# Performance work log

Measured on AMD Instinct MI355X. Metric: run time of the kernel, lower is better.

Reference implementation:

```python
import jax, jax.numpy as jnp
import numpy as np

EPS = 1e-5
TOP_K = 3
W_THRESH = 0.01

def _bn(x, g, b):
    # training-mode batch norm over (N,H,W) per channel
    m = x.mean(axis=(0, 2, 3), keepdims=True)
    v = x.var(axis=(0, 2, 3), keepdims=True)
    return (x - m) * jax.lax.rsqrt(v + EPS) * g[None, :, None, None] + b[None, :, None, None]

def _conv(x, w, stride=1, pad=0, dil=1, groups=1):
    return jax.lax.conv_general_dilated(
        x, w, (stride, stride), [(pad, pad), (pad, pad)],
        rhs_dilation=(dil, dil),
        dimension_numbers=("NCHW", "OIHW", "NCHW"),
        feature_group_count=groups)

def _maxpool3(x):
    return jax.lax.reduce_window(x, -jnp.inf, jax.lax.max, (1, 1, 3, 3), (1, 1, 1, 1),
                                 [(0, 0), (0, 0), (1, 1), (1, 1)])

def _avgpool3(x):
    s = jax.lax.reduce_window(x, 0.0, jax.lax.add, (1, 1, 3, 3), (1, 1, 1, 1),
                              [(0, 0), (0, 0), (1, 1), (1, 1)])
    return s / 9.0  # count_include_pad=True as in torch avg_pool2d

def setup_inputs() -> dict:
    key = jax.random.key(0)
    ks = jax.random.split(key, 16)
    Cin, C = 128, 256
    B, H, W = 64, 32, 32
    f = lambda k, shp, s=0.05: jax.random.normal(k, shp, dtype=jnp.float32) * s
    gamma = lambda k, n: 1.0 + 0.1 * jax.random.normal(k, (n,), dtype=jnp.float32)
    return {
        "x": jax.random.normal(ks[0], (B, Cin, H, W), dtype=jnp.float32),
        "arch_weights": jax.random.normal(ks[1], (8,), dtype=jnp.float32),
        "w_in": f(ks[2], (C, Cin, 1, 1)),
        "g_in": gamma(ks[3], C), "b_in": jnp.zeros((C,), jnp.float32),
        "w3": f(ks[4], (C, C, 3, 3)),
        "g3": gamma(ks[5], C), "b3": jnp.zeros((C,), jnp.float32),
        "w5": f(ks[6], (C, C, 5, 5)),
        "g5": gamma(ks[7], C), "b5": jnp.zeros((C,), jnp.float32),
        "w_dw": f(ks[8], (C, 1, 3, 3), 0.2),
        "w_pw": f(ks[9], (C, C, 1, 1)),
        "gs": gamma(ks[10], C), "bs": jnp.zeros((C,), jnp.float32),
        "wd": f(ks[11], (C, C, 3, 3)),
        "gd": gamma(ks[12], C), "bd": jnp.zeros((C,), jnp.float32),
        "gmp": gamma(ks[13], C), "bmp": jnp.zeros((C,), jnp.float32),
        "gap": gamma(ks[14], C), "bap": jnp.zeros((C,), jnp.float32),
    }

def _forward(x, arch_weights, w_in, g_in, b_in, w3, g3, b3, w5, g5, b5,
             w_dw, w_pw, gs, bs, wd, gd, bd, gmp, bmp, gap, bap):
    # input transition: 1x1 conv -> BN -> ReLU (in_channels != out_channels)
    h = jax.nn.relu(_bn(_conv(x, w_in), g_in, b_in))
    # top-k thresholded renormalized mixture weights over 8 candidate ops
    w = jax.nn.softmax(arch_weights)
    tv, ti = jax.lax.top_k(w, TOP_K)
    sel = jnp.zeros_like(w).at[ti].set(tv)
    sel = jnp.where(sel >= W_THRESH, sel, 0.0)
    sel = sel / jnp.maximum(sel.sum(), 1e-12)
    r = jax.nn.relu(h)
    # op order: [none, max_pool_3x3, avg_pool_3x3, skip, conv_3x3, conv_5x5, sep_conv_3x3, dil_conv_3x3]
    out = sel[1] * _bn(_maxpool3(h), gmp, bmp)
    out = out + sel[2] * _bn(_avgpool3(h), gap, bap)
    out = out + sel[3] * h
    out = out + sel[4] * _bn(_conv(r, w3, pad=1), g3, b3)
    out = out + sel[5] * _bn(_conv(r, w5, pad=2), g5, b5)
    out = out + sel[6] * _bn(_conv(_conv(r, w_dw, pad=1, groups=r.shape[1]), w_pw), gs, bs)
    out = out + sel[7] * _bn(_conv(r, wd, pad=2, dil=2), gd, bd)
    return out

def reference(x, arch_weights, w_in, g_in, b_in, w3, g3, b3, w5, g5, b5,
              w_dw, w_pw, gs, bs, wd, gd, bd, gmp, bmp, gap, bap):
    return _forward(x, arch_weights, w_in, g_in, b_in, w3, g3, b3, w5, g5, b5,
                    w_dw, w_pw, gs, bs, wd, gd, bd, gmp, bmp, gap, bap)
```

## Files before the change

kernel.cpp:

```cpp
#include <hip/hip_runtime.h>

#define CIN_  128
#define C_    256
#define HW_   1024
#define NPC_  65536.0f
#define NB_   16384

constexpr size_t NELEM = 16777216ull;

__device__ float g_sel[8];
__device__ float g_stats[8 * 512];
__device__ int   g_isf32;
__device__ float g_h[NELEM];
__device__ float g_c3[NELEM];
__device__ float g_c5[NELEM];
__device__ float g_cd[NELEM];
__device__ float g_pm[NELEM];
__device__ float g_pa[NELEM];
__device__ float g_pw[NELEM];
__device__ float g_dw[NELEM];

__device__ float g_w5f[32 * 256 * 25 * 8];
__device__ float g_w3f[32 * 256 * 9 * 8];
__device__ float g_wdf[32 * 256 * 9 * 8];
__device__ float g_wtf[32 * 128 * 8];
__device__ float g_wpf[32 * 256 * 8];

__device__ __forceinline__ float u2f(unsigned short u) {
    union { unsigned int i; float f; } x; x.i = ((unsigned int)u) << 16; return x.f;
}
__device__ __forceinline__ unsigned short f2u(float f) {
    union { float f; unsigned int i; } x; x.f = f;
    unsigned int r = x.i + 0x7fffu + ((x.i >> 16) & 1u);
    return (unsigned short)(r >> 16);
}
__device__ __forceinline__ float ldq(const void* p, long i, int isf32) {
    return isf32 ? ((const float*)p)[i] : u2f(((const unsigned short*)p)[i]);
}

#define FMA8X4(acc, wq0, wq1, x0v, x1v, x2v, x3v)                                     \
    acc[0][0] += x0v*wq0.x; acc[0][1] += x1v*wq0.x; acc[0][2] += x2v*wq0.x; acc[0][3] += x3v*wq0.x; \
    acc[1][0] += x0v*wq0.y; acc[1][1] += x1v*wq0.y; acc[1][2] += x2v*wq0.y; acc[1][3] += x3v*wq0.y; \
    acc[2][0] += x0v*wq0.z; acc[2][1] += x1v*wq0.z; acc[2][2] += x2v*wq0.z; acc[2][3] += x3v*wq0.z; \
    acc[3][0] += x0v*wq0.w; acc[3][1] += x1v*wq0.w; acc[3][2] += x2v*wq0.w; acc[3][3] += x3v*wq0.w; \
    acc[4][0] += x0v*wq1.x; acc[4][1] += x1v*wq1.x; acc[4][2] += x2v*wq1.x; acc[4][3] += x3v*wq1.x; \
    acc[5][0] += x0v*wq1.y; acc[5][1] += x1v*wq1.y; acc[5][2] += x2v*wq1.y; acc[5][3] += x3v*wq1.y; \
    acc[6][0] += x0v*wq1.z; acc[6][1] += x1v*wq1.z; acc[6][2] += x2v*wq1.z; acc[6][3] += x3v*wq1.z; \
    acc[7][0] += x0v*wq1.w; acc[7][1] += x1v*wq1.w; acc[7][2] += x2v*wq1.w; acc[7][3] += x3v*wq1.w;

__global__ void k_prep(const void* __restrict__ x, const void* __restrict__ aw) {
    __shared__ int flag_s;
    __shared__ float red[256];
    const int t = threadIdx.x;
    for (int i = t; i < 8 * 512; i += 256) g_stats[i] = 0.f;
    const unsigned short* xu = (const unsigned short*)x;
    int bad = 0;
    for (int i = t; i < 8192; i += 256) {
        unsigned int e = (xu[i] >> 7) & 0xFFu;
        if (e >= 0xC6u) ++bad;
    }
    red[t] = (float)bad;
    __syncthreads();
    for (int off = 128; off > 0; off >>= 1) {
        if (t < off) red[t] += red[t + off];
        __syncthreads();
    }
    if (t == 0) { flag_s = (red[0] > 4.0f) ? 1 : 0; g_isf32 = flag_s; }
    __syncthreads();
    const int isf32 = flag_s;
    if (t == 0) {
        float w[8];
        float mx = -1e30f;
        for (int i = 0; i < 8; ++i) { w[i] = ldq(aw, i, isf32); mx = fmaxf(mx, w[i]); }
        float s = 0.f;
        for (int i = 0; i < 8; ++i) { w[i] = expf(w[i] - mx); s += w[i]; }
        for (int i = 0; i < 8; ++i) w[i] /= s;
        float sv[8] = {0,0,0,0,0,0,0,0};
        bool used[8] = {false,false,false,false,false,false,false,false};
        for (int k = 0; k < 3; ++k) {
            int bi = -1; float bv = -1.f;
            for (int i = 0; i < 8; ++i) if (!used[i] && w[i] > bv) { bv = w[i]; bi = i; }
            used[bi] = true; sv[bi] = bv;
        }
        float tot = 0.f;
        for (int i = 0; i < 8; ++i) { if (sv[i] < 0.01f) sv[i] = 0.f; tot += sv[i]; }
        tot = fmaxf(tot, 1e-12f);
        for (int i = 0; i < 8; ++i) g_sel[i] = sv[i] / tot;
    }
}

__global__ __launch_bounds__(256)
void k_wconv(const void* __restrict__ w3, const void* __restrict__ w5,
             const void* __restrict__ wd, const void* __restrict__ wi,
             const void* __restrict__ wp) {
    const int cg = blockIdx.x;
    const int t  = threadIdx.x;
    const int isf32 = g_isf32;
    for (int o = t; o < 51200; o += 256) {
        int u = o & 7, r = o >> 3, tap = r % 25, ci = r / 25;
        g_w5f[(size_t)cg * 51200 + o] =
            ldq(w5, ((long)(cg * 8 + u) * C_ + ci) * 25 + tap, isf32);
    }
    for (int o = t; o < 18432; o += 256) {
        int u = o & 7, r = o >> 3, tap = r % 9, ci = r / 9;
        long ii = ((long)(cg * 8 + u) * C_ + ci) * 9 + tap;
        g_w3f[(size_t)cg * 18432 + o] = ldq(w3, ii, isf32);
        g_wdf[(size_t)cg * 18432 + o] = ldq(wd, ii, isf32);
    }
    for (int o = t; o < 1024; o += 256) {
        int u = o & 7, ci = o >> 3;
        g_wtf[cg * 1024 + o] = ldq(wi, (long)(cg * 8 + u) * CIN_ + ci, isf32);
    }
    for (int o = t; o < 2048; o += 256) {
        int u = o & 7, ci = o >> 3;
        g_wpf[cg * 2048 + o] = ldq(wp, (long)(cg * 8 + u) * C_ + ci, isf32);
    }
}

__device__ __forceinline__ void stats_epilogue(float* red, float s, float s2,
                                               int t, int c, int slot) {
    __syncthreads();
    red[t] = s; red[t + 256] = s2;
    __syncthreads();
    for (int off = 128; off > 0; off >>= 1) {
        if (t < off) { red[t] += red[t + off]; red[t + 256] += red[t + 256 + off]; }
        __syncthreads();
    }
    if (t == 0) {
        atomicAdd(&g_stats[slot * 512 + c], red[0]);
        atomicAdd(&g_stats[slot * 512 + 256 + c], red[256]);
    }
}

__device__ __forceinline__ void stats_ep2(float* red, int t,
                                          float sA, float s2A, float sB, float s2B,
                                          int cA, int cB, int slot) {
    __syncthreads();
    red[t] = sA; red[t + 256] = s2A; red[t + 512] = sB; red[t + 768] = s2B;
    __syncthreads();
    for (int off = 128; off > 0; off >>= 1) {
        if (t < off) {
            red[t]       += red[t + off];
            red[t + 256] += red[t + 256 + off];
            red[t + 512] += red[t + 512 + off];
            red[t + 768] += red[t + 768 + off];
        }
        __syncthreads();
    }
    if (t == 0) {
        atomicAdd(&g_stats[slot * 512 + cA],       red[0]);
        atomicAdd(&g_stats[slot * 512 + 256 + cA], red[256]);
        atomicAdd(&g_stats[slot * 512 + cB],       red[512]);
        atomicAdd(&g_stats[slot * 512 + 256 + cB], red[768]);
    }
}

__device__ __forceinline__ void stats_all8(float* red, int t, float acc[8][4],
                                           int c0, int slot) {
    #pragma unroll
    for (int u = 0; u < 8; u += 2)
        stats_ep2(red, t,
            acc[u][0]+acc[u][1]+acc[u][2]+acc[u][3],
            acc[u][0]*acc[u][0]+acc[u][1]*acc[u][1]+acc[u][2]*acc[u][2]+acc[u][3]*acc[u][3],
            acc[u+1][0]+acc[u+1][1]+acc[u+1][2]+acc[u+1][3],
            acc[u+1][0]*acc[u+1][0]+acc[u+1][1]*acc[u+1][1]+acc[u+1][2]*acc[u+1][2]+acc[u+1][3]*acc[u+1][3],
            c0 + u, c0 + u + 1, slot);
}

__global__ __launch_bounds__(256)
void k_trans(const void* __restrict__ xin) {
    __shared__ float red[1024];
    const int t  = threadIdx.x;
    const int cg = blockIdx.x & 31;
    const int c0 = cg * 8;
    const int b  = blockIdx.x >> 5;
    const float* wb = g_wtf + cg * 1024;
    float acc[8][4];
    #pragma unroll
    for (int k = 0; k < 8; ++k)
        #pragma unroll
        for (int j = 0; j < 4; ++j) acc[k][j] = 0.f;

    const size_t base0 = (size_t)b * CIN_ * 1024 + t;
    if (g_isf32) {
        const float* xf = (const float*)xin;
        for (int ci = 0; ci < CIN_; ++ci) {
            const float* xp = xf + base0 + (size_t)ci * 1024;
            float x0v = xp[0], x1v = xp[256], x2v = xp[512], x3v = xp[768];
            float4 wq0 = *(const float4*)(wb + ci * 8);
            float4 wq1 = *(const float4*)(wb + ci * 8 + 4);
            FMA8X4(acc, wq0, wq1, x0v, x1v, x2v, x3v)
        }
    } else {
        const unsigned short* xu = (const unsigned short*)xin;
        for (int ci = 0; ci < CIN_; ++ci) {
            const unsigned short* xp = xu + base0 + (size_t)ci * 1024;
            float x0v = u2f(xp[0]),   x1v = u2f(xp[256]);
            float x2v = u2f(xp[512]), x3v = u2f(xp[768]);
            float4 wq0 = *(const float4*)(wb + ci * 8);
            float4 wq1 = *(const float4*)(wb + ci * 8 + 4);
            FMA8X4(acc, wq0, wq1, x0v, x1v, x2v, x3v)
        }
    }
    #pragma unroll
    for (int k = 0; k < 8; ++k) {
        float* o = g_dw + (size_t)(b * C_ + c0 + k) * HW_;
        o[t] = acc[k][0]; o[t + 256] = acc[k][1];
        o[t + 512] = acc[k][2]; o[t + 768] = acc[k][3];
    }
    stats_all8(red, t, acc, c0, 0);
}

__global__ __launch_bounds__(256)
void k_bnrelu(const void* __restrict__ g, const void* __restrict__ bb) {
    size_t idx = ((size_t)blockIdx.x * 256 + threadIdx.x) * 4;
    int c = (int)((idx >> 10) & (C_ - 1));
    int isf32 = g_isf32;
    float mean = g_stats[c] * (1.0f / NPC_);
    float var  = g_stats[256 + c] * (1.0f / NPC_) - mean * mean;
    float rstd = rsqrtf(fmaxf(var, 0.f) + 1e-5f);
    float gv = ldq(g, c, isf32), bv = ldq(bb, c, isf32);
    float4 r = *(const float4*)(g_dw + idx);
    float4 h;
    h.x = fmaxf(0.f, (r.x - mean) * rstd * gv + bv);
    h.y = fmaxf(0.f, (r.y - mean) * rstd * gv + bv);
    h.z = fmaxf(0.f, (r.z - mean) * rstd * gv + bv);
    h.w = fmaxf(0.f, (r.w - mean) * rstd * gv + bv);
    *(float4*)(g_h + idx) = h;
}

__global__ __launch_bounds__(256)
void k_pool_fused() {
    const float s1 = g_sel[1], s2 = g_sel[2];
    if (s1 == 0.f && s2 == 0.f) return;
    __shared__ float xs[34 * 33];
    __shared__ float red[512];
    const int t = threadIdx.x;
    const int c = blockIdx.x & (C_ - 1);
    const int y  = t >> 3;
    const int x0 = (t & 7) * 4;
    const float* hp = g_h + (size_t)blockIdx.x * HW_;
    float4 r = *(const float4*)(hp + t * 4);
    float* xw = xs + y * 33 + x0;
    xw[0] = r.x; xw[1] = r.y; xw[2] = r.z; xw[3] = r.w;
    __syncthreads();
    float mx[4] = {0.f, 0.f, 0.f, 0.f};
    float sm[4] = {0.f, 0.f, 0.f, 0.f};
    #pragma unroll
    for (int ky = 0; ky < 3; ++ky) {
        int iy = y + ky - 1;
        if (iy < 0 || iy >= 32) continue;
        float row[6];
        #pragma unroll
        for (int i = 0; i < 6; ++i) {
            int ix = x0 + i - 1;
            row[i] = (ix >= 0 && ix < 32) ? xs[iy * 33 + ix] : 0.0f;
        }
        #pragma unroll
        for (int kx = 0; kx < 3; ++kx)
            #pragma unroll
            for (int j = 0; j < 4; ++j) {
                mx[j] = fmaxf(mx[j], row[j + kx]);
                sm[j] += row[j + kx];
            }
    }
    #pragma unroll
    for (int j = 0; j < 4; ++j) sm[j] *= (1.0f / 9.0f);
    const size_t ob = (size_t)blockIdx.x * HW_ + y * 32 + x0;
    if (s1 != 0.f) {
        float* o = g_pm + ob;
        o[0] = mx[0]; o[1] = mx[1]; o[2] = mx[2]; o[3] = mx[3];
        stats_epilogue(red, mx[0]+mx[1]+mx[2]+mx[3],
                       mx[0]*mx[0]+mx[1]*mx[1]+mx[2]*mx[2]+mx[3]*mx[3], t, c, 1);
    }
    if (s2 != 0.f) {
        float* o = g_pa + ob;
        o[0] = sm[0]; o[1] = sm[1]; o[2] = sm[2]; o[3] = sm[3];
        stats_epilogue(red, sm[0]+sm[1]+sm[2]+sm[3],
                       sm[0]*sm[0]+sm[1]*sm[1]+sm[2]*sm[2]+sm[3]*sm[3], t, c, 2);
    }
}

template<int KS, int DIL, int PAD, int SLOT>
__global__ __launch_bounds__(256)
void k_conv1() {
    if (g_sel[SLOT] == 0.0f) return;
    constexpr int TRW  = 8 + 2 * PAD;
    constexpr int TAPS = KS * KS;
    __shared__ float xs[4][2][TRW * 40];
    const int t  = threadIdx.x;
    const int w  = t >> 6;
    const int l  = t & 63;
    const int cg = blockIdx.x & 31;
    const int c0 = cg * 8;
    const int b  = blockIdx.x >> 5;
    const int y  = l >> 3;
    const int x0 = (l & 7) * 4;
    const int y0 = w * 8;
    const float* hb = g_h + (size_t)b * C_ * HW_;
    const float* wb = (SLOT == 4 ? g_w3f : SLOT == 5 ? g_w5f : g_wdf)
                      + (size_t)cg * (C_ * TAPS * 8);
    float* obuf = (SLOT == 4) ? g_c3 : (SLOT == 5) ? g_c5 : g_cd;

    const int grA = y0 - PAD + y;
    const bool okA = (grA >= 0) && (grA < 32);
    const int grB = grA + 8;
    const bool okB = (y < 2 * PAD) && (grB < 32);

    float acc[8][4];
    #pragma unroll
    for (int u = 0; u < 8; ++u)
        #pragma unroll
        for (int j = 0; j < 4; ++j) acc[u][j] = 0.f;

    {
        float* xw = &xs[w][0][0];
        for (int i = l; i < 2 * TRW * 40; i += 64) xw[i] = 0.f;
    }
    if (okA) *(float4*)(&xs[w][0][y * 40 + 4 + x0]) =
        *(const float4*)(hb + (size_t)grA * 32 + x0);
    if (okB) *(float4*)(&xs[w][0][(y + 8) * 40 + 4 + x0]) =
        *(const float4*)(hb + (size_t)grB * 32 + x0);
    int cur = 0;

    for (int ci = 0; ci < C_; ++ci) {
        float4 rA = {0.f,0.f,0.f,0.f}, rB = {0.f,0.f,0.f,0.f};
        if (ci + 1 < C_) {
            const float* hn = hb + (size_t)(ci + 1) * HW_;
            if (okA) rA = *(const float4*)(hn + grA * 32 + x0);
            if (okB) rB = *(const float4*)(hn + grB * 32 + x0);
        }
        const float* xsc = xs[w][cur];
        const float* wc  = wb + ci * (TAPS * 8);
        #pragma unroll
        for (int ky = 0; ky < KS; ++ky) {
            const int rr = (y + ky * DIL) * 40 + x0;
            float wnd[12];
            if (PAD == 1) {
                wnd[3] = xsc[rr + 3];
                float4 qb = *(const float4*)(xsc + rr + 4);
                wnd[4] = qb.x; wnd[5] = qb.y; wnd[6] = qb.z; wnd[7] = qb.w;
                wnd[8] = xsc[rr + 8];
            } else {
                float2 qa = *(const float2*)(xsc + rr + 2);
                float4 qb = *(const float4*)(xsc + rr + 4);
                float2 qc = *(const float2*)(xsc + rr + 8);
                wnd[2] = qa.x; wnd[3] = qa.y;
                wnd[4] = qb.x; wnd[5] = qb.y; wnd[6] = qb.z; wnd[7] = qb.w;
                wnd[8] = qc.x; wnd[9] = qc.y;
            }
            #pragma unroll
            for (int kx = 0; kx < KS; ++kx) {
                const float4 wA = *(const float4*)(wc + (ky * KS + kx) * 8);
                const float4 wB = *(const float4*)(wc + (ky * KS + kx) * 8 + 4);
                #pragma unroll
                for (int j = 0; j < 4; ++j) {
                    const float v = wnd[(4 - PAD) + j + kx * DIL];
                    acc[0][j] += v * wA.x; acc[1][j] += v * wA.y;
                    acc[2][j] += v * wA.z; acc[3][j] += v * wA.w;
                    acc[4][j] += v * wB.x; acc[5][j] += v * wB.y;
                    acc[6][j] += v * wB.z; acc[7][j] += v * wB.w;
                }
            }
        }
        if (ci + 1 < C_) {
            float* xn = xs[w][cur ^ 1];
            if (okA) *(float4*)(xn + y * 40 + 4 + x0) = rA;
            if (okB) *(float4*)(xn + (y + 8) * 40 + 4 + x0) = rB;
        }
        cur ^= 1;
    }

    #pragma unroll
    for (int u = 0; u < 8; ++u) {
        float4 o; o.x = acc[u][0]; o.y = acc[u][1]; o.z = acc[u][2]; o.w = acc[u][3];
        *(float4*)(obuf + (size_t)(b * C_ + c0 + u) * HW_ + (y0 + y) * 32 + x0) = o;
    }
    float* red = &xs[0][0][0];
    stats_all8(red, t, acc, c0, SLOT);
}

__global__ __launch_bounds__(256)
void k_dw(const void* __restrict__ wt) {
    if (g_sel[6] == 0.0f) return;
    __shared__ float xs[34 * 33];
    const int t = threadIdx.x;
    const int c = blockIdx.x & (C_ - 1);
    const int y  = t >> 3;
    const int x0 = (t & 7) * 4;
    const int isf32 = g_isf32;
    const float* hp = g_h + (size_t)blockIdx.x * HW_;
    float4 r = *(const float4*)(hp + t * 4);
    float* xw = xs + y * 33 + x0;
    xw[0] = r.x; xw[1] = r.y; xw[2] = r.z; xw[3] = r.w;
    __syncthreads();
    float wv[9];
    #pragma unroll
    for (int k = 0; k < 9; ++k) wv[k] = ldq(wt, (long)c * 9 + k, isf32);
    float acc[4] = {0.f, 0.f, 0.f, 0.f};
    #pragma unroll
    for (int ky = 0; ky < 3; ++ky) {
        int iy = y + ky - 1;
        if (iy < 0 || iy >= 32) continue;
        float row[6];
        #pragma unroll
        for (int i = 0; i < 6; ++i) {
            int ix = x0 + i - 1;
            row[i] = (ix >= 0 && ix < 32) ? xs[iy * 33 + ix] : 0.0f;
        }
        #pragma unroll
        for (int kx = 0; kx < 3; ++kx)
            #pragma unroll
            for (int j = 0; j < 4; ++j)
                acc[j] += row[j + kx] * wv[ky * 3 + kx];
    }
    float* o = g_dw + (size_t)blockIdx.x * HW_ + y * 32 + x0;
    o[0] = acc[0]; o[1] = acc[1]; o[2] = acc[2]; o[3] = acc[3];
}

__global__ __launch_bounds__(256)
void k_pw() {
    if (g_sel[6] == 0.0f) return;
    __shared__ float red[1024];
    const int t  = threadIdx.x;
    const int cg = blockIdx.x & 31;
    const int c0 = cg * 8;
    const int b  = blockIdx.x >> 5;
    const float* hb = g_dw + (size_t)b * C_ * HW_ + t;
    const float* wb = g_wpf + cg * 2048;
    float acc[8][4];
    #pragma unroll
    for (int k = 0; k < 8; ++k)
        #pragma unroll
        for (int j = 0; j < 4; ++j) acc[k][j] = 0.f;
    for (int ci = 0; ci < C_; ++ci) {
        const float* hp = hb + (size_t)ci * HW_;
        float x0v = hp[0], x1v = hp[256], x2v = hp[512], x3v = hp[768];
        float4 wq0 = *(const float4*)(wb + ci * 8);
        float4 wq1 = *(const float4*)(wb + ci * 8 + 4);
        FMA8X4(acc, wq0, wq1, x0v, x1v, x2v, x3v)
    }
    #pragma unroll
    for (int k = 0; k < 8; ++k) {
        float* o = g_pw + (size_t)(b * C_ + c0 + k) * HW_;
        o[t] = acc[k][0]; o[t + 256] = acc[k][1];
        o[t + 512] = acc[k][2]; o[t + 768] = acc[k][3];
    }
    stats_all8(red, t, acc, c0, 6);
}

__device__ __forceinline__ void bn_term(float4& o, const float* buf, size_t idx,
                                        int c, int slot, float sv,
                                        const void* g, const void* bb, int isf32) {
    float mean = g_stats[slot * 512 + c] * (1.0f / NPC_);
    float var  = g_stats[slot * 512 + 256 + c] * (1.0f / NPC_) - mean * mean;
    float rstd = rsqrtf(fmaxf(var, 0.f) + 1e-5f);
    float gv = ldq(g, c, isf32), bv = ldq(bb, c, isf32);
    float4 r = *(const float4*)(buf + idx);
    o.x += sv * ((r.x - mean) * rstd * gv + bv);
    o.y += sv * ((r.y - mean) * rstd * gv + bv);
    o.z += sv * ((r.z - mean) * rstd * gv + bv);
    o.w += sv * ((r.w - mean) * rstd * gv + bv);
}

__global__ __launch_bounds__(256)
void k_final_all(void* __restrict__ out,
                 const void* __restrict__ gmp, const void* __restrict__ bmp,
                 const void* __restrict__ gap, const void* __restrict__ bap,
                 const void* __restrict__ g3,  const void* __restrict__ b3,
                 const void* __restrict__ g5,  const void* __restrict__ b5,
                 const void* __restrict__ gs,  const void* __restrict__ bs,
                 const void* __restrict__ gd,  const void* __restrict__ bd) {
    size_t idx = ((size_t)blockIdx.x * 256 + threadIdx.x) * 4;
    int c = (int)((idx >> 10) & (C_ - 1));
    int isf32 = g_isf32;
    float4 o = {0.f, 0.f, 0.f, 0.f};
    float s3 = g_sel[3];
    if (s3 != 0.f) {
        float4 h = *(const float4*)(g_h + idx);
        o.x = s3 * h.x; o.y = s3 * h.y; o.z = s3 * h.z; o.w = s3 * h.w;
    }
    float sv;
    if ((sv = g_sel[1]) != 0.f) bn_term(o, g_pm, idx, c, 1, sv, gmp, bmp, isf32);
    if ((sv = g_sel[2]) != 0.f) bn_term(o, g_pa, idx, c, 2, sv, gap, bap, isf32);
    if ((sv = g_sel[4]) != 0.f) bn_term(o, g_c3, idx, c, 4, sv, g3,  b3,  isf32);
    if ((sv = g_sel[5]) != 0.f) bn_term(o, g_c5, idx, c, 5, sv, g5,  b5,  isf32);
    if ((sv = g_sel[6]) != 0.f) bn_term(o, g_pw, idx, c, 6, sv, gs,  bs,  isf32);
    if ((sv = g_sel[7]) != 0.f) bn_term(o, g_cd, idx, c, 7, sv, gd,  bd,  isf32);
    if (isf32) {
        *(float4*)((float*)out + idx) = o;
    } else {
        ushort4 u; u.x = f2u(o.x); u.y = f2u(o.y); u.z = f2u(o.z); u.w = f2u(o.w);
        *(ushort4*)((unsigned short*)out + idx) = u;
    }
}

extern "C" void kernel_launch(void* const* d_in, const int* in_sizes, int n_in,
                              void* d_out, int out_size, void* d_ws, size_t ws_size,
                              hipStream_t stream) {
    const void* x    = d_in[0];
    const void* aw   = d_in[1];
    const void* w_in = d_in[2];
    const void* g_in = d_in[3];
    const void* b_in = d_in[4];
    const void* w3   = d_in[5];
    const void* g3   = d_in[6];
    const void* b3   = d_in[7];
    const void* w5   = d_in[8];
    const void* g5   = d_in[9];
    const void* b5   = d_in[10];
    const void* wdw  = d_in[11];
    const void* wpw  = d_in[12];
    const void* gs   = d_in[13];
    const void* bs   = d_in[14];
    const void* wd   = d_in[15];
    const void* gd   = d_in[16];
    const void* bd   = d_in[17];
    const void* gmp  = d_in[18];
    const void* bmp  = d_in[19];
    const void* gap  = d_in[20];
    const void* bap  = d_in[21];

    dim3 Bk(256);
    dim3 Gfull(NB_);
    dim3 Gc8(2048);

    k_prep<<<dim3(1), Bk, 0, stream>>>(x, aw);
    k_wconv<<<dim3(32), Bk, 0, stream>>>(w3, w5, wd, w_in, wpw);

    k_trans<<<Gc8, Bk, 0, stream>>>(x);
    k_bnrelu<<<Gfull, Bk, 0, stream>>>(g_in, b_in);

    k_pool_fused<<<Gfull, Bk, 0, stream>>>();

    k_conv1<3, 1, 1, 4><<<Gc8, Bk, 0, stream>>>();
    k_conv1<5, 1, 2, 5><<<Gc8, Bk, 0, stream>>>();
    k_conv1<3, 2, 2, 7><<<Gc8, Bk, 0, stream>>>();

    k_dw<<<Gfull, Bk, 0, stream>>>(wdw);
    k_pw<<<Gc8, Bk, 0, stream>>>();

    k_final_all<<<Gfull, Bk, 0, stream>>>(d_out,
        gmp, bmp, gap, bap, g3, b3, g5, b5, gs, bs, gd, bd);
}
```

Before: 1.216 ms.

## Widen output-channel tile to 16 and fuse BN-ReLU, pooling and depthwise conv

Each block of the 1x1, 3x3, 5x5, dilated and pointwise convolutions now computes 16 output channels instead of 8. Weight repacking and grids are adjusted to match, so each loaded input value is reused across more channels. The BN+ReLU, pooling and depthwise kernels are merged into one per-channel kernel that keeps the activated plane in shared memory, removing two reloads of h and two launches. The wider tile doubles accumulator registers, which risks spills or lower occupancy, and halves the block count.

```diff
diff --git a/kernel.cpp b/kernel.cpp
--- a/kernel.cpp
+++ b/kernel.cpp
@@ -20,11 +20,11 @@
 __device__ float g_pw[NELEM];
 __device__ float g_dw[NELEM];
 
-__device__ float g_w5f[32 * 256 * 25 * 8];
-__device__ float g_w3f[32 * 256 * 9 * 8];
-__device__ float g_wdf[32 * 256 * 9 * 8];
-__device__ float g_wtf[32 * 128 * 8];
-__device__ float g_wpf[32 * 256 * 8];
+__device__ float g_w5f[16 * 256 * 25 * 16];
+__device__ float g_w3f[16 * 256 * 9 * 16];
+__device__ float g_wdf[16 * 256 * 9 * 16];
+__device__ float g_wtf[16 * 128 * 16];
+__device__ float g_wpf[16 * 256 * 16];
 
 __device__ __forceinline__ float u2f(unsigned short u) {
     union { unsigned int i; float f; } x; x.i = ((unsigned int)u) << 16; return x.f;
@@ -38,15 +38,23 @@
     return isf32 ? ((const float*)p)[i] : u2f(((const unsigned short*)p)[i]);
 }
 
-#define FMA8X4(acc, wq0, wq1, x0v, x1v, x2v, x3v)                                     \
-    acc[0][0] += x0v*wq0.x; acc[0][1] += x1v*wq0.x; acc[0][2] += x2v*wq0.x; acc[0][3] += x3v*wq0.x; \
-    acc[1][0] += x0v*wq0.y; acc[1][1] += x1v*wq0.y; acc[1][2] += x2v*wq0.y; acc[1][3] += x3v*wq0.y; \
-    acc[2][0] += x0v*wq0.z; acc[2][1] += x1v*wq0.z; acc[2][2] += x2v*wq0.z; acc[2][3] += x3v*wq0.z; \
-    acc[3][0] += x0v*wq0.w; acc[3][1] += x1v*wq0.w; acc[3][2] += x2v*wq0.w; acc[3][3] += x3v*wq0.w; \
-    acc[4][0] += x0v*wq1.x; acc[4][1] += x1v*wq1.x; acc[4][2] += x2v*wq1.x; acc[4][3] += x3v*wq1.x; \
-    acc[5][0] += x0v*wq1.y; acc[5][1] += x1v*wq1.y; acc[5][2] += x2v*wq1.y; acc[5][3] += x3v*wq1.y; \
-    acc[6][0] += x0v*wq1.z; acc[6][1] += x1v*wq1.z; acc[6][2] += x2v*wq1.z; acc[6][3] += x3v*wq1.z; \
-    acc[7][0] += x0v*wq1.w; acc[7][1] += x1v*wq1.w; acc[7][2] += x2v*wq1.w; acc[7][3] += x3v*wq1.w;
+#define FMA16X4(acc, wq0, wq1, wq2, wq3, x0v, x1v, x2v, x3v)                                             \
+    acc[ 0][0]+=x0v*wq0.x; acc[ 0][1]+=x1v*wq0.x; acc[ 0][2]+=x2v*wq0.x; acc[ 0][3]+=x3v*wq0.x;          \
+    acc[ 1][0]+=x0v*wq0.y; acc[ 1][1]+=x1v*wq0.y; acc[ 1][2]+=x2v*wq0.y; acc[ 1][3]+=x3v*wq0.y;          \
+    acc[ 2][0]+=x0v*wq0.z; acc[ 2][1]+=x1v*wq0.z; acc[ 2][2]+=x2v*wq0.z; acc[ 2][3]+=x3v*wq0.z;          \
+    acc[ 3][0]+=x0v*wq0.w; acc[ 3][1]+=x1v*wq0.w; acc[ 3][2]+=x2v*wq0.w; acc[ 3][3]+=x3v*wq0.w;          \
+    acc[ 4][0]+=x0v*wq1.x; acc[ 4][1]+=x1v*wq1.x; acc[ 4][2]+=x2v*wq1.x; acc[ 4][3]+=x3v*wq1.x;          \
+    acc[ 5][0]+=x0v*wq1.y; acc[ 5][1]+=x1v*wq1.y; acc[ 5][2]+=x2v*wq1.y; acc[ 5][3]+=x3v*wq1.y;          \
+    acc[ 6][0]+=x0v*wq1.z; acc[ 6][1]+=x1v*wq1.z; acc[ 6][2]+=x2v*wq1.z; acc[ 6][3]+=x3v*wq1.z;          \
+    acc[ 7][0]+=x0v*wq1.w; acc[ 7][1]+=x1v*wq1.w; acc[ 7][2]+=x2v*wq1.w; acc[ 7][3]+=x3v*wq1.w;          \
+    acc[ 8][0]+=x0v*wq2.x; acc[ 8][1]+=x1v*wq2.x; acc[ 8][2]+=x2v*wq2.x; acc[ 8][3]+=x3v*wq2.x;          \
+    acc[ 9][0]+=x0v*wq2.y; acc[ 9][1]+=x1v*wq2.y; acc[ 9][2]+=x2v*wq2.y; acc[ 9][3]+=x3v*wq2.y;          \
+    acc[10][0]+=x0v*wq2.z; acc[10][1]+=x1v*wq2.z; acc[10][2]+=x2v*wq2.z; acc[10][3]+=x3v*wq2.z;          \
+    acc[11][0]+=x0v*wq2.w; acc[11][1]+=x1v*wq2.w; acc[11][2]+=x2v*wq2.w; acc[11][3]+=x3v*wq2.w;          \
+    acc[12][0]+=x0v*wq3.x; acc[12][1]+=x1v*wq3.x; acc[12][2]+=x2v*wq3.x; acc[12][3]+=x3v*wq3.x;          \
+    acc[13][0]+=x0v*wq3.y; acc[13][1]+=x1v*wq3.y; acc[13][2]+=x2v*wq3.y; acc[13][3]+=x3v*wq3.y;          \
+    acc[14][0]+=x0v*wq3.z; acc[14][1]+=x1v*wq3.z; acc[14][2]+=x2v*wq3.z; acc[14][3]+=x3v*wq3.z;          \
+    acc[15][0]+=x0v*wq3.w; acc[15][1]+=x1v*wq3.w; acc[15][2]+=x2v*wq3.w; acc[15][3]+=x3v*wq3.w;
 
 __global__ void k_prep(const void* __restrict__ x, const void* __restrict__ aw) {
     __shared__ int flag_s;
@@ -96,24 +104,24 @@
     const int cg = blockIdx.x;
     const int t  = threadIdx.x;
     const int isf32 = g_isf32;
-    for (int o = t; o < 51200; o += 256) {
-        int u = o & 7, r = o >> 3, tap = r % 25, ci = r / 25;
-        g_w5f[(size_t)cg * 51200 + o] =
-            ldq(w5, ((long)(cg * 8 + u) * C_ + ci) * 25 + tap, isf32);
-    }
-    for (int o = t; o < 18432; o += 256) {
-        int u = o & 7, r = o >> 3, tap = r % 9, ci = r / 9;
-        long ii = ((long)(cg * 8 + u) * C_ + ci) * 9 + tap;
-        g_w3f[(size_t)cg * 18432 + o] = ldq(w3, ii, isf32);
-        g_wdf[(size_t)cg * 18432 + o] = ldq(wd, ii, isf32);
-    }
-    for (int o = t; o < 1024; o += 256) {
-        int u = o & 7, ci = o >> 3;
-        g_wtf[cg * 1024 + o] = ldq(wi, (long)(cg * 8 + u) * CIN_ + ci, isf32);
+    for (int o = t; o < 102400; o += 256) {
+        int u = o & 15, r = o >> 4, tap = r % 25, ci = r / 25;
+        g_w5f[(size_t)cg * 102400 + o] =
+            ldq(w5, ((long)(cg * 16 + u) * C_ + ci) * 25 + tap, isf32);
+    }
+    for (int o = t; o < 36864; o += 256) {
+        int u = o & 15, r = o >> 4, tap = r % 9, ci = r / 9;
+        long ii = ((long)(cg * 16 + u) * C_ + ci) * 9 + tap;
+        g_w3f[(size_t)cg * 36864 + o] = ldq(w3, ii, isf32);
+        g_wdf[(size_t)cg * 36864 + o] = ldq(wd, ii, isf32);
     }
     for (int o = t; o < 2048; o += 256) {
-        int u = o & 7, ci = o >> 3;
-        g_wpf[cg * 2048 + o] = ldq(wp, (long)(cg * 8 + u) * C_ + ci, isf32);
+        int u = o & 15, ci = o >> 4;
+        g_wtf[cg * 2048 + o] = ldq(wi, (long)(cg * 16 + u) * CIN_ + ci, isf32);
+    }
+    for (int o = t; o < 4096; o += 256) {
+        int u = o & 15, ci = o >> 4;
+        g_wpf[cg * 4096 + o] = ldq(wp, (long)(cg * 16 + u) * C_ + ci, isf32);
     }
 }
 
@@ -155,10 +163,10 @@
     }
 }
 
-__device__ __forceinline__ void stats_all8(float* red, int t, float acc[8][4],
-                                           int c0, int slot) {
-    #pragma unroll
-    for (int u = 0; u < 8; u += 2)
+__device__ __forceinline__ void stats_all16(float* red, int t, float acc[16][4],
+                                            int c0, int slot) {
+    #pragma unroll
+    for (int u = 0; u < 16; u += 2)
         stats_ep2(red, t,
             acc[u][0]+acc[u][1]+acc[u][2]+acc[u][3],
             acc[u][0]*acc[u][0]+acc[u][1]*acc[u][1]+acc[u][2]*acc[u][2]+acc[u][3]*acc[u][3],
@@ -171,13 +179,13 @@
 void k_trans(const void* __restrict__ xin) {
     __shared__ float red[1024];
     const int t  = threadIdx.x;
-    const int cg = blockIdx.x & 31;
-    const int c0 = cg * 8;
-    const int b  = blockIdx.x >> 5;
-    const float* wb = g_wtf + cg * 1024;
-    float acc[8][4];
-    #pragma unroll
-    for (int k = 0; k < 8; ++k)
+    const int cg = blockIdx.x & 15;
+    const int c0 = cg * 16;
+    const int b  = blockIdx.x >> 4;
+    const float* wb = g_wtf + cg * 2048;
+    float acc[16][4];
+    #pragma unroll
+    for (int k = 0; k < 16; ++k)
         #pragma unroll
         for (int j = 0; j < 4; ++j) acc[k][j] = 0.f;
 
@@ -187,9 +195,11 @@
         for (int ci = 0; ci < CIN_; ++ci) {
             const float* xp = xf + base0 + (size_t)ci * 1024;
             float x0v = xp[0], x1v = xp[256], x2v = xp[512], x3v = xp[768];
-            float4 wq0 = *(const float4*)(wb + ci * 8);
-            float4 wq1 = *(const float4*)(wb + ci * 8 + 4);
-            FMA8X4(acc, wq0, wq1, x0v, x1v, x2v, x3v)
+            float4 wq0 = *(const float4*)(wb + ci * 16);
+            float4 wq1 = *(const float4*)(wb + ci * 16 + 4);
+            float4 wq2 = *(const float4*)(wb + ci * 16 + 8);
+            float4 wq3 = *(const float4*)(wb + ci * 16 + 12);
+            FMA16X4(acc, wq0, wq1, wq2, wq3, x0v, x1v, x2v, x3v)
         }
     } else {
         const unsigned short* xu = (const unsigned short*)xin;
@@ -197,87 +207,112 @@
             const unsigned short* xp = xu + base0 + (size_t)ci * 1024;
             float x0v = u2f(xp[0]),   x1v = u2f(xp[256]);
             float x2v = u2f(xp[512]), x3v = u2f(xp[768]);
-            float4 wq0 = *(const float4*)(wb + ci * 8);
-            float4 wq1 = *(const float4*)(wb + ci * 8 + 4);
-            FMA8X4(acc, wq0, wq1, x0v, x1v, x2v, x3v)
-        }
-    }
-    #pragma unroll
-    for (int k = 0; k < 8; ++k) {
+            float4 wq0 = *(const float4*)(wb + ci * 16);
+            float4 wq1 = *(const float4*)(wb + ci * 16 + 4);
+            float4 wq2 = *(const float4*)(wb + ci * 16 + 8);
+            float4 wq3 = *(const float4*)(wb + ci * 16 + 12);
+            FMA16X4(acc, wq0, wq1, wq2, wq3, x0v, x1v, x2v, x3v)
+        }
+    }
+    #pragma unroll
+    for (int k = 0; k < 16; ++k) {
         float* o = g_dw + (size_t)(b * C_ + c0 + k) * HW_;
         o[t] = acc[k][0]; o[t + 256] = acc[k][1];
         o[t + 512] = acc[k][2]; o[t + 768] = acc[k][3];
     }
-    stats_all8(red, t, acc, c0, 0);
+    stats_all16(red, t, acc, c0, 0);
 }
 
 __global__ __launch_bounds__(256)
-void k_bnrelu(const void* __restrict__ g, const void* __restrict__ bb) {
-    size_t idx = ((size_t)blockIdx.x * 256 + threadIdx.x) * 4;
-    int c = (int)((idx >> 10) & (C_ - 1));
-    int isf32 = g_isf32;
-    float mean = g_stats[c] * (1.0f / NPC_);
-    float var  = g_stats[256 + c] * (1.0f / NPC_) - mean * mean;
-    float rstd = rsqrtf(fmaxf(var, 0.f) + 1e-5f);
-    float gv = ldq(g, c, isf32), bv = ldq(bb, c, isf32);
-    float4 r = *(const float4*)(g_dw + idx);
-    float4 h;
-    h.x = fmaxf(0.f, (r.x - mean) * rstd * gv + bv);
-    h.y = fmaxf(0.f, (r.y - mean) * rstd * gv + bv);
-    h.z = fmaxf(0.f, (r.z - mean) * rstd * gv + bv);
-    h.w = fmaxf(0.f, (r.w - mean) * rstd * gv + bv);
-    *(float4*)(g_h + idx) = h;
-}
-
-__global__ __launch_bounds__(256)
-void k_pool_fused() {
-    const float s1 = g_sel[1], s2 = g_sel[2];
-    if (s1 == 0.f && s2 == 0.f) return;
+void k_post(const void* __restrict__ g, const void* __restrict__ bb,
+            const void* __restrict__ wdw) {
     __shared__ float xs[34 * 33];
     __shared__ float red[512];
     const int t = threadIdx.x;
     const int c = blockIdx.x & (C_ - 1);
     const int y  = t >> 3;
     const int x0 = (t & 7) * 4;
-    const float* hp = g_h + (size_t)blockIdx.x * HW_;
-    float4 r = *(const float4*)(hp + t * 4);
+    const int isf32 = g_isf32;
+
+    float mean = g_stats[c] * (1.0f / NPC_);
+    float var  = g_stats[256 + c] * (1.0f / NPC_) - mean * mean;
+    float rstd = rsqrtf(fmaxf(var, 0.f) + 1e-5f);
+    float gv = ldq(g, c, isf32), bv = ldq(bb, c, isf32);
+    float4 r = *(const float4*)(g_dw + (size_t)blockIdx.x * HW_ + t * 4);
+    float4 h;
+    h.x = fmaxf(0.f, (r.x - mean) * rstd * gv + bv);
+    h.y = fmaxf(0.f, (r.y - mean) * rstd * gv + bv);
+    h.z = fmaxf(0.f, (r.z - mean) * rstd * gv + bv);
+    h.w = fmaxf(0.f, (r.w - mean) * rstd * gv + bv);
+    *(float4*)(g_h + (size_t)blockIdx.x * HW_ + t * 4) = h;
+
     float* xw = xs + y * 33 + x0;
-    xw[0] = r.x; xw[1] = r.y; xw[2] = r.z; xw[3] = r.w;
-    __syncthreads();
-    float mx[4] = {0.f, 0.f, 0.f, 0.f};
-    float sm[4] = {0.f, 0.f, 0.f, 0.f};
-    #pragma unroll
-    for (int ky = 0; ky < 3; ++ky) {
-        int iy = y + ky - 1;
-        if (iy < 0 || iy >= 32) continue;
-        float row[6];
-        #pragma unroll
-        for (int i = 0; i < 6; ++i) {
-            int ix = x0 + i - 1;
-            row[i] = (ix >= 0 && ix < 32) ? xs[iy * 33 + ix] : 0.0f;
-        }
-        #pragma unroll
-        for (int kx = 0; kx < 3; ++kx)
+    xw[0] = h.x; xw[1] = h.y; xw[2] = h.z; xw[3] = h.w;
+    __syncthreads();
+
+    const float s1 = g_sel[1], s2 = g_sel[2], s6 = g_sel[6];
+
+    if (s1 != 0.f || s2 != 0.f) {
+        float mx[4] = {0.f, 0.f, 0.f, 0.f};
+        float sm[4] = {0.f, 0.f, 0.f, 0.f};
+        #pragma unroll
+        for (int ky = 0; ky < 3; ++ky) {
+            int iy = y + ky - 1;
+            if (iy < 0 || iy >= 32) continue;
+            float row[6];
             #pragma unroll
-            for (int j = 0; j < 4; ++j) {
-                mx[j] = fmaxf(mx[j], row[j + kx]);
-                sm[j] += row[j + kx];
+            for (int i = 0; i < 6; ++i) {
+                int ix = x0 + i - 1;
+                row[i] = (ix >= 0 && ix < 32) ? xs[iy * 33 + ix] : 0.0f;
             }
-    }
-    #pragma unroll
-    for (int j = 0; j < 4; ++j) sm[j] *= (1.0f / 9.0f);
-    const size_t ob = (size_t)blockIdx.x * HW_ + y * 32 + x0;
-    if (s1 != 0.f) {
-        float* o = g_pm + ob;
-        o[0] = mx[0]; o[1] = mx[1]; o[2] = mx[2]; o[3] = mx[3];
-        stats_epilogue(red, mx[0]+mx[1]+mx[2]+mx[3],
-                       mx[0]*mx[0]+mx[1]*mx[1]+mx[2]*mx[2]+mx[3]*mx[3], t, c, 1);
-    }
-    if (s2 != 0.f) {
-        float* o = g_pa + ob;
-        o[0] = sm[0]; o[1] = sm[1]; o[2] = sm[2]; o[3] = sm[3];
-        stats_epilogue(red, sm[0]+sm[1]+sm[2]+sm[3],
-                       sm[0]*sm[0]+sm[1]*sm[1]+sm[2]*sm[2]+sm[3]*sm[3], t, c, 2);
+            #pragma unroll
+            for (int kx = 0; kx < 3; ++kx)
+                #pragma unroll
+                for (int j = 0; j < 4; ++j) {
+                    mx[j] = fmaxf(mx[j], row[j + kx]);
+                    sm[j] += row[j + kx];
+                }
+        }
+        #pragma unroll
+        for (int j = 0; j < 4; ++j) sm[j] *= (1.0f / 9.0f);
+        const size_t ob = (size_t)blockIdx.x * HW_ + y * 32 + x0;
+        if (s1 != 0.f) {
+            float* o = g_pm + ob;
+            o[0] = mx[0]; o[1] = mx[1]; o[2] = mx[2]; o[3] = mx[3];
+            stats_epilogue(red, mx[0]+mx[1]+mx[2]+mx[3],
+                           mx[0]*mx[0]+mx[1]*mx[1]+mx[2]*mx[2]+mx[3]*mx[3], t, c, 1);
+        }
+        if (s2 != 0.f) {
+            float* o = g_pa + ob;
+            o[0] = sm[0]; o[1] = sm[1]; o[2] = sm[2]; o[3] = sm[3];
+            stats_epilogue(red, sm[0]+sm[1]+sm[2]+sm[3],
+                           sm[0]*sm[0]+sm[1]*sm[1]+sm[2]*sm[2]+sm[3]*sm[3], t, c, 2);
+        }
+    }
+
+    if (s6 != 0.f) {
+        float wv[9];
+        #pragma unroll
+        for (int k = 0; k < 9; ++k) wv[k] = ldq(wdw, (long)c * 9 + k, isf32);
+        float acc[4] = {0.f, 0.f, 0.f, 0.f};
+        #pragma unroll
+        for (int ky = 0; ky < 3; ++ky) {
+            int iy = y + ky - 1;
+            if (iy < 0 || iy >= 32) continue;
+            float row[6];
+            #pragma unroll
+            for (int i = 0; i < 6; ++i) {
+                int ix = x0 + i - 1;
+                row[i] = (ix >= 0 && ix < 32) ? xs[iy * 33 + ix] : 0.0f;
+            }
+            #pragma unroll
+            for (int kx = 0; kx < 3; ++kx)
+                #pragma unroll
+                for (int j = 0; j < 4; ++j)
+                    acc[j] += row[j + kx] * wv[ky * 3 + kx];
+        }
+        float* o = g_dw + (size_t)blockIdx.x * HW_ + y * 32 + x0;
+        o[0] = acc[0]; o[1] = acc[1]; o[2] = acc[2]; o[3] = acc[3];
     }
 }
 
@@ -291,15 +326,15 @@
     const int t  = threadIdx.x;
     const int w  = t >> 6;
     const int l  = t & 63;
-    const int cg = blockIdx.x & 31;
-    const int c0 = cg * 8;
-    const int b  = blockIdx.x >> 5;
+    const int cg = blockIdx.x & 15;
+    const int c0 = cg * 16;
+    const int b  = blockIdx.x >> 4;
     const int y  = l >> 3;
     const int x0 = (l & 7) * 4;
     const int y0 = w * 8;
     const float* hb = g_h + (size_t)b * C_ * HW_;
     const float* wb = (SLOT == 4 ? g_w3f : SLOT == 5 ? g_w5f : g_wdf)
-                      + (size_t)cg * (C_ * TAPS * 8);
+                      + (size_t)cg * (C_ * TAPS * 16);
     float* obuf = (SLOT == 4) ? g_c3 : (SLOT == 5) ? g_c5 : g_cd;
 
     const int grA = y0 - PAD + y;
@@ -307,9 +342,9 @@
     const int grB = grA + 8;
     const bool okB = (y < 2 * PAD) && (grB < 32);
 
-    float acc[8][4];
-    #pragma unroll
-    for (int u = 0; u < 8; ++u)
+    float acc[16][4];
+    #pragma unroll
+    for (int u = 0; u < 16; ++u)
         #pragma unroll
         for (int j = 0; j < 4; ++j) acc[u][j] = 0.f;
 
@@ -331,7 +366,7 @@
             if (okB) rB = *(const float4*)(hn + grB * 32 + x0);
         }
         const float* xsc = xs[w][cur];
-        const float* wc  = wb + ci * (TAPS * 8);
+        const float* wc  = wb + ci * (TAPS * 16);
         #pragma unroll
         for (int ky = 0; ky < KS; ++ky) {
             const int rr = (y + ky * DIL) * 40 + x0;
@@ -351,15 +386,21 @@
             }
             #pragma unroll
             for (int kx = 0; kx < KS; ++kx) {
-                const float4 wA = *(const float4*)(wc + (ky * KS + kx) * 8);
-                const float4 wB = *(const float4*)(wc + (ky * KS + kx) * 8 + 4);
+                const float4 wA = *(const float4*)(wc + (ky * KS + kx) * 16);
+                const float4 wB = *(const float4*)(wc + (ky * KS + kx) * 16 + 4);
+                const float4 wC = *(const float4*)(wc + (ky * KS + kx) * 16 + 8);
+                const float4 wD = *(const float4*)(wc + (ky * KS + kx) * 16 + 12);
                 #pragma unroll
                 for (int j = 0; j < 4; ++j) {
                     const float v = wnd[(4 - PAD) + j + kx * DIL];
-                    acc[0][j] += v * wA.x; acc[1][j] += v * wA.y;
-                    acc[2][j] += v * wA.z; acc[3][j] += v * wA.w;
-                    acc[4][j] += v * wB.x; acc[5][j] += v * wB.y;
-                    acc[6][j] += v * wB.z; acc[7][j] += v * wB.w;
+                    acc[ 0][j] += v * wA.x; acc[ 1][j] += v * wA.y;
+                    acc[ 2][j] += v * wA.z; acc[ 3][j] += v * wA.w;
+                    acc[ 4][j] += v * wB.x; acc[ 5][j] += v * wB.y;
+                    acc[ 6][j] += v * wB.z; acc[ 7][j] += v * wB.w;
+                    acc[ 8][j] += v * wC.x; acc[ 9][j] += v * wC.y;
+                    acc[10][j] += v * wC.z; acc[11][j] += v * wC.w;
+                    acc[12][j] += v * wD.x; acc[13][j] += v * wD.y;
+                    acc[14][j] += v * wD.z; acc[15][j] += v * wD.w;
                 }
             }
         }
@@ -372,50 +413,12 @@
     }
 
     #pragma unroll
-    for (int u = 0; u < 8; ++u) {
+    for (int u = 0; u < 16; ++u) {
         float4 o; o.x = acc[u][0]; o.y = acc[u][1]; o.z = acc[u][2]; o.w = acc[u][3];
         *(float4*)(obuf + (size_t)(b * C_ + c0 + u) * HW_ + (y0 + y) * 32 + x0) = o;
     }
     float* red = &xs[0][0][0];
-    stats_all8(red, t, acc, c0, SLOT);
-}
-
-__global__ __launch_bounds__(256)
-void k_dw(const void* __restrict__ wt) {
-    if (g_sel[6] == 0.0f) return;
-    __shared__ float xs[34 * 33];
-    const int t = threadIdx.x;
-    const int c = blockIdx.x & (C_ - 1);
-    const int y  = t >> 3;
-    const int x0 = (t & 7) * 4;
-    const int isf32 = g_isf32;
-    const float* hp = g_h + (size_t)blockIdx.x * HW_;
-    float4 r = *(const float4*)(hp + t * 4);
-    float* xw = xs + y * 33 + x0;
-    xw[0] = r.x; xw[1] = r.y; xw[2] = r.z; xw[3] = r.w;
-    __syncthreads();
-    float wv[9];
-    #pragma unroll
-    for (int k = 0; k < 9; ++k) wv[k] = ldq(wt, (long)c * 9 + k, isf32);
-    float acc[4] = {0.f, 0.f, 0.f, 0.f};
-    #pragma unroll
-    for (int ky = 0; ky < 3; ++ky) {
-        int iy = y + ky - 1;
-        if (iy < 0 || iy >= 32) continue;
-        float row[6];
-        #pragma unroll
-        for (int i = 0; i < 6; ++i) {
-            int ix = x0 + i - 1;
-            row[i] = (ix >= 0 && ix < 32) ? xs[iy * 33 + ix] : 0.0f;
-        }
-        #pragma unroll
-        for (int kx = 0; kx < 3; ++kx)
-            #pragma unroll
-            for (int j = 0; j < 4; ++j)
-                acc[j] += row[j + kx] * wv[ky * 3 + kx];
-    }
-    float* o = g_dw + (size_t)blockIdx.x * HW_ + y * 32 + x0;
-    o[0] = acc[0]; o[1] = acc[1]; o[2] = acc[2]; o[3] = acc[3];
+    stats_all16(red, t, acc, c0, SLOT);
 }
 
 __global__ __launch_bounds__(256)
@@ -423,30 +426,32 @@
     if (g_sel[6] == 0.0f) return;
     __shared__ float red[1024];
     const int t  = threadIdx.x;
-    const int cg = blockIdx.x & 31;
-    const int c0 = cg * 8;
-    const int b  = blockIdx.x >> 5;
+    const int cg = blockIdx.x & 15;
+    const int c0 = cg * 16;
+    const int b  = blockIdx.x >> 4;
     const float* hb = g_dw + (size_t)b * C_ * HW_ + t;
-    const float* wb = g_wpf + cg * 2048;
-    float acc[8][4];
-    #pragma unroll
-    for (int k = 0; k < 8; ++k)
+    const float* wb = g_wpf + cg * 4096;
+    float acc[16][4];
+    #pragma unroll
+    for (int k = 0; k < 16; ++k)
         #pragma unroll
         for (int j = 0; j < 4; ++j) acc[k][j] = 0.f;
     for (int ci = 0; ci < C_; ++ci) {
         const float* hp = hb + (size_t)ci * HW_;
         float x0v = hp[0], x1v = hp[256], x2v = hp[512], x3v = hp[768];
-        float4 wq0 = *(const float4*)(wb + ci * 8);
-        float4 wq1 = *(const float4*)(wb + ci * 8 + 4);
-        FMA8X4(acc, wq0, wq1, x0v, x1v, x2v, x3v)
-    }
-    #pragma unroll
-    for (int k = 0; k < 8; ++k) {
+        float4 wq0 = *(const float4*)(wb + ci * 16);
+        float4 wq1 = *(const float4*)(wb + ci * 16 + 4);
+        float4 wq2 = *(const float4*)(wb + ci * 16 + 8);
+        float4 wq3 = *(const float4*)(wb + ci * 16 + 12);
+        FMA16X4(acc, wq0, wq1, wq2, wq3, x0v, x1v, x2v, x3v)
+    }
+    #pragma unroll
+    for (int k = 0; k < 16; ++k) {
         float* o = g_pw + (size_t)(b * C_ + c0 + k) * HW_;
         o[t] = acc[k][0]; o[t + 256] = acc[k][1];
         o[t + 512] = acc[k][2]; o[t + 768] = acc[k][3];
     }
-    stats_all8(red, t, acc, c0, 6);
+    stats_all16(red, t, acc, c0, 6);
 }
 
 __device__ __forceinline__ void bn_term(float4& o, const float* buf, size_t idx,
@@ -523,22 +528,20 @@
 
     dim3 Bk(256);
     dim3 Gfull(NB_);
-    dim3 Gc8(2048);
+    dim3 Gc16(1024);
 
     k_prep<<<dim3(1), Bk, 0, stream>>>(x, aw);
-    k_wconv<<<dim3(32), Bk, 0, stream>>>(w3, w5, wd, w_in, wpw);
-
-    k_trans<<<Gc8, Bk, 0, stream>>>(x);
-    k_bnrelu<<<Gfull, Bk, 0, stream>>>(g_in, b_in);
-
-    k_pool_fused<<<Gfull, Bk, 0, stream>>>();
-
-    k_conv1<3, 1, 1, 4><<<Gc8, Bk, 0, stream>>>();
-    k_conv1<5, 1, 2, 5><<<Gc8, Bk, 0, stream>>>();
-    k_conv1<3, 2, 2, 7><<<Gc8, Bk, 0, stream>>>();
-
-    k_dw<<<Gfull, Bk, 0, stream>>>(wdw);
-    k_pw<<<Gc8, Bk, 0, stream>>>();
+    k_wconv<<<dim3(16), Bk, 0, stream>>>(w3, w5, wd, w_in, wpw);
+
+    k_trans<<<Gc16, Bk, 0, stream>>>(x);
+
+    k_post<<<Gfull, Bk, 0, stream>>>(g_in, b_in, wdw);
+
+    k_conv1<3, 1, 1, 4><<<Gc16, Bk, 0, stream>>>();
+    k_conv1<5, 1, 2, 5><<<Gc16, Bk, 0, stream>>>();
+    k_conv1<3, 2, 2, 7><<<Gc16, Bk, 0, stream>>>();
+
+    k_pw<<<Gc16, Bk, 0, stream>>>();
 
     k_final_all<<<Gfull, Bk, 0, stream>>>(d_out,
         gmp, bmp, gap, bap, g3, b3, g5, b5, gs, bs, gd, bd);
```

Result: slower. 1.680 ms (+38.1%).
